# Performance work log

Hardware: AMD Instinct MI355X
Metric: run time of the kernel (lower is better)

The kernel has to match this reference:

```python
import jax, jax.numpy as jnp
import numpy as np

D_MODEL = 1024
N_HEAD = 16
ATT_DIM = D_MODEL // N_HEAD


def setup_inputs() -> dict:
    key = jax.random.key(0)
    ks = jax.random.split(key, 7)
    B, S = 2, 2048
    q = jax.random.normal(ks[0], (B, S, D_MODEL), dtype=jnp.float32)
    k = jax.random.normal(ks[1], (B, S, D_MODEL), dtype=jnp.float32)
    v = jax.random.normal(ks[2], (B, S, D_MODEL), dtype=jnp.float32)
    # per-head projection weights, stored as [H, d_model, att_dim] (x @ W form)
    scale_qkv = float(np.sqrt(6.0 / (D_MODEL + ATT_DIM)))  # xavier_uniform
    Wq = jax.random.uniform(ks[3], (N_HEAD, D_MODEL, ATT_DIM), jnp.float32, -scale_qkv, scale_qkv)
    Wk = jax.random.uniform(ks[4], (N_HEAD, D_MODEL, ATT_DIM), jnp.float32, -scale_qkv, scale_qkv)
    Wv = jax.random.uniform(ks[5], (N_HEAD, D_MODEL, ATT_DIM), jnp.float32, -scale_qkv, scale_qkv)
    scale_o = float(np.sqrt(6.0 / (D_MODEL + D_MODEL)))
    Wo = jax.random.uniform(ks[6], (D_MODEL, D_MODEL), jnp.float32, -scale_o, scale_o)
    return {"q": q, "k": k, "v": v, "Wq": Wq, "Wk": Wk, "Wv": Wv, "Wo": Wo}


def reference(q, k, v, Wq, Wk, Wv, Wo):
    # per-head projections, batched over heads: [H,B,S,E]
    qh = jnp.einsum('bsd,hde->hbse', q, Wq)
    kh = jnp.einsum('bsd,hde->hbse', k, Wk)
    vh = jnp.einsum('bsd,hde->hbse', v, Wv)
    # NOTE: original divides by att_dim (not sqrt(att_dim))
    scores = jnp.einsum('hbqe,hbke->hbqk', qh, kh) / ATT_DIM
    attn = jax.nn.softmax(scores, axis=-1)  # [H,B,Sq,Sk]
    att = jnp.einsum('hbqk,hbke->hbqe', attn, vh)  # [H,B,S,E]
    # concat heads along last dim in head order, then output projection
    H, B, S, E = att.shape
    cat = jnp.transpose(att, (1, 2, 0, 3)).reshape(B, S, H * E)
    out = cat @ Wo  # dropout is identity in eval
    return (out, attn)
```

## Files before the change

### kernel.cpp

```cpp
#include <hip/hip_runtime.h>
#include <hip/hip_bf16.h>

#define DM 1024
#define NH 16
#define AD 64
#define BB 2
#define SS 2048
#define LOG2E 1.44269504f

typedef float f32x4 __attribute__((ext_vector_type(4)));
typedef short bf16x8 __attribute__((ext_vector_type(8)));
typedef unsigned short u16;
typedef unsigned int u32;
typedef u16 u16x4 __attribute__((ext_vector_type(4)));
typedef u16 u16x8 __attribute__((ext_vector_type(8)));
typedef u32 u32x4 __attribute__((ext_vector_type(4)));

static __device__ __forceinline__ u16 f2bf(float f) {
  unsigned u = __builtin_bit_cast(unsigned, f);
  u += 0x7fffu + ((u >> 16) & 1u);
  return (u16)(u >> 16);
}

#define MFMA16(a, b, c) __builtin_amdgcn_mfma_f32_16x16x32_bf16((a), (b), (c), 0, 0, 0)

static __device__ __forceinline__ void ld_lds16(const void* g, void* l) {
  __builtin_amdgcn_global_load_lds((const __attribute__((address_space(1))) u32*)g,
                                   (__attribute__((address_space(3))) u32*)l, 16, 0, 0);
}

#define WAITV(N)                                             \
  do {                                                       \
    asm volatile("s_waitcnt vmcnt(" #N ")" ::: "memory");    \
    __builtin_amdgcn_sched_barrier(0);                       \
  } while (0)
#define WAITL0()                                             \
  do {                                                       \
    asm volatile("s_waitcnt lgkmcnt(0)" ::: "memory");       \
    __builtin_amdgcn_sched_barrier(0);                       \
  } while (0)
#define BAR() __builtin_amdgcn_s_barrier()

#define KFRAG(buf, row, P) (*(const bf16x8*)(&(buf)[(row) * 64 + ((((P) ^ ((row) & 7))) << 3)]))
#define V64(buf, row, P, hh) \
  (*(const u16x4*)(&(buf)[(row) * 64 + ((((P) ^ ((row) & 7))) << 3) + (hh) * 4]))

static __device__ __forceinline__ u32 cvt_pk_bf16(float lo, float hi) {
  u32 r;
  asm("v_cvt_pk_bf16_f32 %0, %1, %2" : "=v"(r) : "v"(lo), "v"(hi));
  return r;
}

__global__ __launch_bounds__(256, 4) void cast3_kernel(const float* __restrict__ s0,
                                                       const float* __restrict__ s1,
                                                       const float* __restrict__ s2,
                                                       u16* __restrict__ d0, u16* __restrict__ d1,
                                                       u16* __restrict__ d2, int n8) {
  const float* src = blockIdx.y == 0 ? s0 : blockIdx.y == 1 ? s1 : s2;
  u16* dst = blockIdx.y == 0 ? d0 : blockIdx.y == 1 ? d1 : d2;
  int i = blockIdx.x * blockDim.x + threadIdx.x;
  int stride = gridDim.x * blockDim.x;
  for (; i < n8; i += stride) {
    const f32x4* p = (const f32x4*)src + 2 * (size_t)i;
    f32x4 a = p[0], b = p[1];
    u16x8 o;
    o[0] = f2bf(a[0]); o[1] = f2bf(a[1]); o[2] = f2bf(a[2]); o[3] = f2bf(a[3]);
    o[4] = f2bf(b[0]); o[5] = f2bf(b[1]); o[6] = f2bf(b[2]); o[7] = f2bf(b[3]);
    *((u16x8*)dst + i) = o;
  }
}

template <int MODE>
__global__ __launch_bounds__(256, 4) void tcast_kernel(const float* __restrict__ s0,
                                                       const float* __restrict__ s1,
                                                       const float* __restrict__ s2,
                                                       u16* __restrict__ dst, int R, int C,
                                                       float scale0) {
  __shared__ float T[64][65];
  const float* src;
  u16* dstp;
  float scale;
  long bo;
  if (MODE == 0) {
    src = s0; bo = (long)blockIdx.z * R * C; dstp = dst; scale = scale0;
  } else {
    int which = blockIdx.z >> 4, zz = blockIdx.z & 15;
    src = which == 0 ? s0 : which == 1 ? s1 : s2;
    bo = (long)zz * R * C;
    dstp = dst + (long)which * NH * R * C;
    scale = which == 0 ? scale0 : 1.0f;
  }
  int r0 = blockIdx.x * 64, c0 = blockIdx.y * 64;
  int cl = threadIdx.x & 63, rl = threadIdx.x >> 6;
#pragma unroll
  for (int i = 0; i < 16; i++) {
    int rr = rl + 4 * i;
    T[cl][rr] = src[bo + (long)(r0 + rr) * C + c0 + cl];
  }
  __syncthreads();
#pragma unroll
  for (int i = 0; i < 16; i++) {
    int cc = rl + 4 * i;
    dstp[bo + (long)(c0 + cc) * R + r0 + cl] = f2bf(T[cc][cl] * scale);
  }
}

__global__ __launch_bounds__(256, 3) void qkvproj_kernel(const u16* __restrict__ X0,
                                                         const u16* __restrict__ WT0,
                                                         u16* __restrict__ out0) {
  __shared__ u16 Ab[2][128 * 64];
  __shared__ u16 Bb[2][64 * 64];
  const long NX = (long)BB * SS * DM;
  const long NW = (long)NH * DM * AD;
  int which = blockIdx.z;
  int sg0 = blockIdx.x * 128;
  int b = sg0 >> 11, s0 = sg0 & (SS - 1);
  int h = blockIdx.y;
  int tid = threadIdx.x, w = tid >> 6, lane = tid & 63, g = lane >> 4, li = lane & 15;
  const u16* xb = X0 + (long)which * NX + ((long)b * SS + s0) * DM;
  const u16* wb = WT0 + (long)which * NW + (long)h * 64 * DM;
  u16* outp = out0 + (long)which * NX;

  const u16* asrc[4];
  u16* adst[2][4];
#pragma unroll
  for (int i = 0; i < 4; i++) {
    int cc = i * 256 + tid;
    int row = cc >> 3, sp = (cc ^ (row & 7)) & 7;
    asrc[i] = xb + (long)row * DM + sp * 8;
    adst[0][i] = &Ab[0][cc * 8];
    adst[1][i] = &Ab[1][cc * 8];
  }
  const u16* bsrc[2];
  u16* bdst[2][2];
#pragma unroll
  for (int i = 0; i < 2; i++) {
    int cc = i * 256 + tid;
    int row = cc >> 3, sp = (cc ^ (row & 7)) & 7;
    bsrc[i] = wb + (long)row * DM + sp * 8;
    bdst[0][i] = &Bb[0][cc * 8];
    bdst[1][i] = &Bb[1][cc * 8];
  }

#pragma unroll
  for (int i = 0; i < 4; i++) ld_lds16(asrc[i], adst[0][i]);
#pragma unroll
  for (int i = 0; i < 2; i++) ld_lds16(bsrc[i], bdst[0][i]);

  f32x4 acc[2][4] = {};
  for (int kc = 0; kc < DM / 64; kc++) {
    int cur = kc & 1;
    if (kc + 1 < DM / 64) {
      int ko = (kc + 1) * 64;
#pragma unroll
      for (int i = 0; i < 4; i++) ld_lds16(asrc[i] + ko, adst[cur ^ 1][i]);
#pragma unroll
      for (int i = 0; i < 2; i++) ld_lds16(bsrc[i] + ko, bdst[cur ^ 1][i]);
      WAITV(6);
    } else {
      WAITV(0);
    }
    BAR();
    const u16* ab = Ab[cur];
    const u16* bb = Bb[cur];
    __builtin_amdgcn_s_setprio(1);
#pragma unroll
    for (int kk = 0; kk < 2; kk++) {
      bf16x8 bf[4];
#pragma unroll
      for (int j = 0; j < 4; j++) bf[j] = KFRAG(bb, j * 16 + li, kk * 4 + g);
#pragma unroll
      for (int mi = 0; mi < 2; mi++) {
        bf16x8 af = KFRAG(ab, w * 32 + mi * 16 + li, kk * 4 + g);
#pragma unroll
        for (int j = 0; j < 4; j++) acc[mi][j] = MFMA16(af, bf[j], acc[mi][j]);
      }
    }
    __builtin_amdgcn_s_setprio(0);
    WAITL0();
    BAR();
  }

  long obase = (long)h * (BB * SS * AD) + (long)b * (SS * AD);
#pragma unroll
  for (int mi = 0; mi < 2; mi++) {
    int sb = s0 + w * 32 + mi * 16 + 4 * g;
#pragma unroll
    for (int j = 0; j < 4; j++) {
      int e = j * 16 + li;
      if (which < 2) {
#pragma unroll
        for (int r = 0; r < 4; r++)
          outp[obase + (long)(sb + r) * AD + e] = f2bf(acc[mi][j][r]);
      } else {
        u16x4 vv;
#pragma unroll
        for (int r = 0; r < 4; r++) vv[r] = f2bf(acc[mi][j][r]);
        *(u16x4*)(outp + obase + (long)e * SS + sb) = vv;
      }
    }
  }
}

__global__ __launch_bounds__(256, 3) void outproj_kernel(const u16* __restrict__ X,
                                                         const u16* __restrict__ WT,
                                                         float* __restrict__ out) {
  __shared__ u16 Ab[2][128 * 64];
  __shared__ u16 Bb[2][64 * 64];
  int sg0 = blockIdx.x * 128;
  int n0 = blockIdx.y * 64;
  int tid = threadIdx.x, w = tid >> 6, lane = tid & 63, g = lane >> 4, li = lane & 15;
  const u16* xb = X + (long)sg0 * DM;
  const u16* wb = WT + (long)n0 * DM;

  const u16* asrc[4];
  u16* adst[2][4];
#pragma unroll
  for (int i = 0; i < 4; i++) {
    int cc = i * 256 + tid;
    int row = cc >> 3, sp = (cc ^ (row & 7)) & 7;
    asrc[i] = xb + (long)row * DM + sp * 8;
    adst[0][i] = &Ab[0][cc * 8];
    adst[1][i] = &Ab[1][cc * 8];
  }
  const u16* bsrc[2];
  u16* bdst[2][2];
#pragma unroll
  for (int i = 0; i < 2; i++) {
    int cc = i * 256 + tid;
    int row = cc >> 3, sp = (cc ^ (row & 7)) & 7;
    bsrc[i] = wb + (long)row * DM + sp * 8;
    bdst[0][i] = &Bb[0][cc * 8];
    bdst[1][i] = &Bb[1][cc * 8];
  }

#pragma unroll
  for (int i = 0; i < 4; i++) ld_lds16(asrc[i], adst[0][i]);
#pragma unroll
  for (int i = 0; i < 2; i++) ld_lds16(bsrc[i], bdst[0][i]);

  f32x4 acc[2][4] = {};
  for (int kc = 0; kc < DM / 64; kc++) {
    int cur = kc & 1;
    if (kc + 1 < DM / 64) {
      int ko = (kc + 1) * 64;
#pragma unroll
      for (int i = 0; i < 4; i++) ld_lds16(asrc[i] + ko, adst[cur ^ 1][i]);
#pragma unroll
      for (int i = 0; i < 2; i++) ld_lds16(bsrc[i] + ko, bdst[cur ^ 1][i]);
      WAITV(6);
    } else {
      WAITV(0);
    }
    BAR();
    const u16* ab = Ab[cur];
    const u16* bb = Bb[cur];
    __builtin_amdgcn_s_setprio(1);
#pragma unroll
    for (int kk = 0; kk < 2; kk++) {
      bf16x8 bf[4];
#pragma unroll
      for (int j = 0; j < 4; j++) bf[j] = KFRAG(bb, j * 16 + li, kk * 4 + g);
#pragma unroll
      for (int mi = 0; mi < 2; mi++) {
        bf16x8 af = KFRAG(ab, w * 32 + mi * 16 + li, kk * 4 + g);
#pragma unroll
        for (int j = 0; j < 4; j++) acc[mi][j] = MFMA16(af, bf[j], acc[mi][j]);
      }
    }
    __builtin_amdgcn_s_setprio(0);
    WAITL0();
    BAR();
  }

#pragma unroll
  for (int mi = 0; mi < 2; mi++) {
    int sb = sg0 + w * 32 + mi * 16 + 4 * g;
#pragma unroll
    for (int j = 0; j < 4; j++) {
      int col = n0 + j * 16 + li;
#pragma unroll
      for (int r = 0; r < 4; r++) out[(long)(sb + r) * DM + col] = acc[mi][j][r];
    }
  }
}

__global__ __launch_bounds__(256, 4) void attn_kernel(const u16* __restrict__ qh,
                                                      const u16* __restrict__ kh,
                                                      const u16* __restrict__ vhT,
                                                      float* __restrict__ attn_out,
                                                      u16* __restrict__ cat) {
  __shared__ u16 Kb[2][64 * 64];
  __shared__ u16 Vb[2][64 * 64];
  int h = blockIdx.y, b = blockIdx.z;
  int hb = h * BB + b;
  int tid = threadIdx.x;
  int w = tid >> 6, lane = tid & 63;
  int g = lane >> 4, li = lane & 15;
  long base = (long)hb * SS * AD;
  const u16* qhb = qh + base;
  const u16* khb = kh + base;
  const u16* vhb = vhT + base;
  int q0 = blockIdx.x * 64 + w * 16;

  bf16x8 bq0 = *(const bf16x8*)(qhb + (q0 + li) * AD + 8 * g);
  bf16x8 bq1 = *(const bf16x8*)(qhb + (q0 + li) * AD + 32 + 8 * g);

  int r1 = tid >> 3, p1 = (tid ^ (r1 & 7)) & 7;
  int r2 = (tid + 256) >> 3, p2 = ((tid + 256) ^ (r2 & 7)) & 7;
  const u16* ks1 = khb + (long)r1 * AD + p1 * 8;
  const u16* ks2 = khb + (long)r2 * AD + p2 * 8;
  const u16* vs1 = vhb + (long)r1 * SS + p1 * 8;
  const u16* vs2 = vhb + (long)r2 * SS + p2 * 8;
  u16* kd0a = &Kb[0][tid * 8]; u16* kd0b = &Kb[0][(tid + 256) * 8];
  u16* kd1a = &Kb[1][tid * 8]; u16* kd1b = &Kb[1][(tid + 256) * 8];
  u16* vd0a = &Vb[0][tid * 8]; u16* vd0b = &Vb[0][(tid + 256) * 8];
  u16* vd1a = &Vb[1][tid * 8]; u16* vd1b = &Vb[1][(tid + 256) * 8];

  float l_run = 0.f;
  ld_lds16(ks1, kd0a); ld_lds16(ks2, kd0b);
  ld_lds16(ks1 + 64 * AD, kd1a); ld_lds16(ks2 + 64 * AD, kd1b);
  ld_lds16(ks1 + 2 * 64 * AD, vd0a); ld_lds16(ks2 + 2 * 64 * AD, vd0b);
  for (int ch4 = 0; ch4 < SS / 64; ch4 += 4) {
#pragma unroll
    for (int u = 0; u < 4; u++) {
      int ch = ch4 + u;
      int slot = (u + 3) & 3;
      u16* pa = slot == 0 ? kd0a : slot == 1 ? kd1a : slot == 2 ? vd0a : vd1a;
      u16* pb = slot == 0 ? kd0b : slot == 1 ? kd1b : slot == 2 ? vd0b : vd1b;
      if (ch + 3 < SS / 64) {
        ld_lds16(ks1 + (ch + 3) * 64 * AD, pa);
        ld_lds16(ks2 + (ch + 3) * 64 * AD, pb);
        WAITV(6);
      } else if (ch == SS / 64 - 3) {
        WAITV(4);
      } else if (ch == SS / 64 - 2) {
        WAITV(2);
      } else {
        WAITV(0);
      }
      BAR();
      const u16* kb = u == 0 ? Kb[0] : u == 1 ? Kb[1] : u == 2 ? Vb[0] : Vb[1];
      f32x4 sacc[4] = {};
      __builtin_amdgcn_s_setprio(1);
#pragma unroll
      for (int mi = 0; mi < 4; mi++) {
        bf16x8 a0 = KFRAG(kb, mi * 16 + li, g);
        bf16x8 a1 = KFRAG(kb, mi * 16 + li, 4 + g);
        sacc[mi] = MFMA16(a0, bq0, sacc[mi]);
        sacc[mi] = MFMA16(a1, bq1, sacc[mi]);
      }
      __builtin_amdgcn_s_setprio(0);
#pragma unroll
      for (int c = 0; c < 4; c++)
#pragma unroll
        for (int r = 0; r < 4; r++) l_run += exp2f(sacc[c][r]);
      WAITL0();
      BAR();
    }
  }
  l_run += __shfl_xor(l_run, 16);
  l_run += __shfl_xor(l_run, 32);
  float moff = log2f(l_run);
  f32x4 minit = {-moff, -moff, -moff, -moff};

  ld_lds16(ks1, kd0a); ld_lds16(ks2, kd0b);
  ld_lds16(vs1, vd0a); ld_lds16(vs2, vd0b);
  f32x4 accv[4] = {};
  float* arow = attn_out + ((long)hb * SS + q0 + li) * SS;
  for (int ch2 = 0; ch2 < SS / 64; ch2 += 2) {
#pragma unroll
    for (int u = 0; u < 2; u++) {
      int ch = ch2 + u;
      u16* kpa = u ? kd0a : kd1a; u16* kpb = u ? kd0b : kd1b;
      u16* vpa = u ? vd0a : vd1a; u16* vpb = u ? vd0b : vd1b;
      if (ch + 1 < SS / 64) {
        ld_lds16(ks1 + (ch + 1) * 64 * AD, kpa);
        ld_lds16(ks2 + (ch + 1) * 64 * AD, kpb);
        ld_lds16(vs1 + (ch + 1) * 64, vpa);
        ld_lds16(vs2 + (ch + 1) * 64, vpb);
        if (ch == 0) {
          WAITV(4);
        } else {
          WAITV(8);
        }
      } else {
        WAITV(4);
      }
      BAR();
      const u16* kb = Kb[u];
      const u16* vb = Vb[u];
      f32x4 sacc[4] = {minit, minit, minit, minit};
      __builtin_amdgcn_s_setprio(1);
#pragma unroll
      for (int mi = 0; mi < 4; mi++) {
        bf16x8 a0 = KFRAG(kb, mi * 16 + li, g);
        bf16x8 a1 = KFRAG(kb, mi * 16 + li, 4 + g);
        sacc[mi] = MFMA16(a0, bq0, sacc[mi]);
        sacc[mi] = MFMA16(a1, bq1, sacc[mi]);
      }
      __builtin_amdgcn_s_setprio(0);
      u32 pw[8];
#pragma unroll
      for (int c = 0; c < 4; c++) {
        f32x4 pv;
#pragma unroll
        for (int r = 0; r < 4; r++) pv[r] = exp2f(sacc[c][r]);
        __builtin_nontemporal_store(pv, (f32x4*)(arow + ch * 64 + c * 16 + 4 * g));
        pw[2 * c] = cvt_pk_bf16(pv[0], pv[1]);
        pw[2 * c + 1] = cvt_pk_bf16(pv[2], pv[3]);
      }
#pragma unroll
      for (int kk = 0; kk < 2; kk++) {
        u32x4 aw = {pw[4 * kk], pw[4 * kk + 1], pw[4 * kk + 2], pw[4 * kk + 3]};
        bf16x8 ap = __builtin_bit_cast(bf16x8, aw);
#pragma unroll
        for (int et = 0; et < 4; et++) {
          int row = et * 16 + li;
          u16x4 b0 = V64(vb, row, 4 * kk + (g >> 1), g & 1);
          u16x4 b1 = V64(vb, row, 4 * kk + 2 + (g >> 1), g & 1);
          u16x8 ub = {b0[0], b0[1], b0[2], b0[3], b1[0], b1[1], b1[2], b1[3]};
          bf16x8 bv = __builtin_bit_cast(bf16x8, ub);
          accv[et] = MFMA16(ap, bv, accv[et]);
        }
      }
      WAITL0();
      BAR();
    }
  }

#pragma unroll
  for (int et = 0; et < 4; et++)
#pragma unroll
    for (int r = 0; r < 4; r++)
      cat[((long)b * SS + q0 + 4 * g + r) * DM + h * AD + et * 16 + li] = f2bf(accv[et][r]);
}

extern "C" void kernel_launch(void* const* d_in, const int* in_sizes, int n_in, void* d_out,
                              int out_size, void* d_ws, size_t ws_size, hipStream_t stream) {
  const float* q = (const float*)d_in[0];
  const float* k = (const float*)d_in[1];
  const float* v = (const float*)d_in[2];
  const float* Wq = (const float*)d_in[3];
  const float* Wk = (const float*)d_in[4];
  const float* Wv = (const float*)d_in[5];
  const float* Wo = (const float*)d_in[6];
  float* out = (float*)d_out;
  float* attn_out = out + (long)BB * SS * DM;

  const long NX = (long)BB * SS * DM;
  const long NW = (long)NH * DM * AD;
  u16* ws = (u16*)d_ws;
  u16* xq = ws;
  u16* xk = xq + NX;
  u16* xv = xk + NX;
  u16* WqT = xv + NX;
  u16* WkT = WqT + NW;
  u16* WvT = WkT + NW;
  u16* WoT = WvT + NW;
  u16* qhw = WoT + (long)DM * DM;
  u16* khw = qhw + NX;
  u16* vhw = khw + NX;
  u16* catw = vhw + NX;

  (void)xk; (void)xv; (void)WkT; (void)WvT;

  cast3_kernel<<<dim3(700, 3), 256, 0, stream>>>(q, k, v, xq, xk, xv, (int)(NX / 8));
  tcast_kernel<1><<<dim3(16, 1, 48), 256, 0, stream>>>(Wq, Wk, Wv, WqT, DM, AD, LOG2E / AD);
  tcast_kernel<0><<<dim3(16, 16, 1), 256, 0, stream>>>(Wo, nullptr, nullptr, WoT, DM, DM, 1.0f);

  qkvproj_kernel<<<dim3(BB * SS / 128, NH, 3), 256, 0, stream>>>(xq, WqT, qhw);

  attn_kernel<<<dim3(SS / 64, NH, BB), 256, 0, stream>>>(qhw, khw, vhw, attn_out, catw);

  outproj_kernel<<<dim3(BB * SS / 128, DM / 64), 256, 0, stream>>>(catw, WoT, out);
}
```

Baseline: 260.5 us.

## Fuse prep kernels, reorder attention grid, split sum accumulators, drop nontemporal stores

Merges the three input-cast and weight-transpose launches into one prep kernel that picks its work from the flat block index, removing two launches. The attention grid now puts head*batch in x and query tile in y, so blocks that run at the same time share K/V for the same head. The softmax-denominator sum uses four independent accumulators to shorten the dependency chain. The attention-probability stores become ordinary stores instead of nontemporal ones, which changes cache behaviour for the large output write.

```diff
diff --git a/kernel.cpp b/kernel.cpp
--- a/kernel.cpp
+++ b/kernel.cpp
@@ -51,47 +51,59 @@
   return r;
 }
 
-__global__ __launch_bounds__(256, 4) void cast3_kernel(const float* __restrict__ s0,
-                                                       const float* __restrict__ s1,
-                                                       const float* __restrict__ s2,
-                                                       u16* __restrict__ d0, u16* __restrict__ d1,
-                                                       u16* __restrict__ d2, int n8) {
-  const float* src = blockIdx.y == 0 ? s0 : blockIdx.y == 1 ? s1 : s2;
-  u16* dst = blockIdx.y == 0 ? d0 : blockIdx.y == 1 ? d1 : d2;
-  int i = blockIdx.x * blockDim.x + threadIdx.x;
-  int stride = gridDim.x * blockDim.x;
-  for (; i < n8; i += stride) {
-    const f32x4* p = (const f32x4*)src + 2 * (size_t)i;
-    f32x4 a = p[0], b = p[1];
-    u16x8 o;
-    o[0] = f2bf(a[0]); o[1] = f2bf(a[1]); o[2] = f2bf(a[2]); o[3] = f2bf(a[3]);
-    o[4] = f2bf(b[0]); o[5] = f2bf(b[1]); o[6] = f2bf(b[2]); o[7] = f2bf(b[3]);
-    *((u16x8*)dst + i) = o;
-  }
-}
-
-template <int MODE>
-__global__ __launch_bounds__(256, 4) void tcast_kernel(const float* __restrict__ s0,
-                                                       const float* __restrict__ s1,
-                                                       const float* __restrict__ s2,
-                                                       u16* __restrict__ dst, int R, int C,
-                                                       float scale0) {
+__global__ __launch_bounds__(256, 4) void prep_kernel(const float* __restrict__ q,
+                                                      const float* __restrict__ k,
+                                                      const float* __restrict__ v,
+                                                      const float* __restrict__ Wq,
+                                                      const float* __restrict__ Wk,
+                                                      const float* __restrict__ Wv,
+                                                      const float* __restrict__ Wo,
+                                                      u16* __restrict__ xq,
+                                                      u16* __restrict__ WqT,
+                                                      u16* __restrict__ WoT) {
   __shared__ float T[64][65];
+  const long NX = (long)BB * SS * DM;
+  int id = blockIdx.x;
+  int tid = threadIdx.x;
+  if (id < 2100) {
+    int tensor = id / 700, xi = id - tensor * 700;
+    const float* src = tensor == 0 ? q : tensor == 1 ? k : v;
+    u16* dst = xq + (long)tensor * NX;
+    int n8 = (int)(NX / 8);
+    int stride = 700 * 256;
+    for (int i = xi * 256 + tid; i < n8; i += stride) {
+      const f32x4* p = (const f32x4*)src + 2 * (size_t)i;
+      f32x4 a = p[0], b = p[1];
+      u16x8 o;
+      o[0] = f2bf(a[0]); o[1] = f2bf(a[1]); o[2] = f2bf(a[2]); o[3] = f2bf(a[3]);
+      o[4] = f2bf(b[0]); o[5] = f2bf(b[1]); o[6] = f2bf(b[2]); o[7] = f2bf(b[3]);
+      *((u16x8*)dst + i) = o;
+    }
+    return;
+  }
   const float* src;
   u16* dstp;
   float scale;
   long bo;
-  if (MODE == 0) {
-    src = s0; bo = (long)blockIdx.z * R * C; dstp = dst; scale = scale0;
+  int R, C, r0, c0;
+  if (id < 2868) {
+    int flat = id - 2100;
+    int x = flat & 15, z = flat >> 4;
+    int which = z >> 4, zz = z & 15;
+    src = which == 0 ? Wq : which == 1 ? Wk : Wv;
+    R = DM; C = AD;
+    bo = (long)zz * R * C;
+    dstp = WqT + (long)which * NH * R * C;
+    scale = which == 0 ? (LOG2E / AD) : 1.0f;
+    r0 = x * 64; c0 = 0;
   } else {
-    int which = blockIdx.z >> 4, zz = blockIdx.z & 15;
-    src = which == 0 ? s0 : which == 1 ? s1 : s2;
-    bo = (long)zz * R * C;
-    dstp = dst + (long)which * NH * R * C;
-    scale = which == 0 ? scale0 : 1.0f;
-  }
-  int r0 = blockIdx.x * 64, c0 = blockIdx.y * 64;
-  int cl = threadIdx.x & 63, rl = threadIdx.x >> 6;
+    int flat = id - 2868;
+    int x = flat & 15, yb = flat >> 4;
+    src = Wo; dstp = WoT; scale = 1.0f;
+    R = DM; C = DM; bo = 0;
+    r0 = x * 64; c0 = yb * 64;
+  }
+  int cl = tid & 63, rl = tid >> 6;
 #pragma unroll
   for (int i = 0; i < 16; i++) {
     int rr = rl + 4 * i;
@@ -292,8 +304,8 @@
                                                       u16* __restrict__ cat) {
   __shared__ u16 Kb[2][64 * 64];
   __shared__ u16 Vb[2][64 * 64];
-  int h = blockIdx.y, b = blockIdx.z;
-  int hb = h * BB + b;
+  int hb = blockIdx.x;
+  int h = hb >> 1, b = hb & 1;
   int tid = threadIdx.x;
   int w = tid >> 6, lane = tid & 63;
   int g = lane >> 4, li = lane & 15;
@@ -301,7 +313,7 @@
   const u16* qhb = qh + base;
   const u16* khb = kh + base;
   const u16* vhb = vhT + base;
-  int q0 = blockIdx.x * 64 + w * 16;
+  int q0 = blockIdx.y * 64 + w * 16;
 
   bf16x8 bq0 = *(const bf16x8*)(qhb + (q0 + li) * AD + 8 * g);
   bf16x8 bq1 = *(const bf16x8*)(qhb + (q0 + li) * AD + 32 + 8 * g);
@@ -317,7 +329,7 @@
   u16* vd0a = &Vb[0][tid * 8]; u16* vd0b = &Vb[0][(tid + 256) * 8];
   u16* vd1a = &Vb[1][tid * 8]; u16* vd1b = &Vb[1][(tid + 256) * 8];
 
-  float l_run = 0.f;
+  f32x4 l4 = {0.f, 0.f, 0.f, 0.f};
   ld_lds16(ks1, kd0a); ld_lds16(ks2, kd0b);
   ld_lds16(ks1 + 64 * AD, kd1a); ld_lds16(ks2 + 64 * AD, kd1b);
   ld_lds16(ks1 + 2 * 64 * AD, vd0a); ld_lds16(ks2 + 2 * 64 * AD, vd0b);
@@ -354,11 +366,12 @@
 #pragma unroll
       for (int c = 0; c < 4; c++)
 #pragma unroll
-        for (int r = 0; r < 4; r++) l_run += exp2f(sacc[c][r]);
+        for (int r = 0; r < 4; r++) l4[r] += exp2f(sacc[c][r]);
       WAITL0();
       BAR();
     }
   }
+  float l_run = (l4[0] + l4[1]) + (l4[2] + l4[3]);
   l_run += __shfl_xor(l_run, 16);
   l_run += __shfl_xor(l_run, 32);
   float moff = log2f(l_run);
@@ -406,7 +419,7 @@
         f32x4 pv;
 #pragma unroll
         for (int r = 0; r < 4; r++) pv[r] = exp2f(sacc[c][r]);
-        __builtin_nontemporal_store(pv, (f32x4*)(arow + ch * 64 + c * 16 + 4 * g));
+        *(f32x4*)(arow + ch * 64 + c * 16 + 4 * g) = pv;
         pw[2 * c] = cvt_pk_bf16(pv[0], pv[1]);
         pw[2 * c + 1] = cvt_pk_bf16(pv[2], pv[3]);
       }
@@ -465,13 +478,11 @@
 
   (void)xk; (void)xv; (void)WkT; (void)WvT;
 
-  cast3_kernel<<<dim3(700, 3), 256, 0, stream>>>(q, k, v, xq, xk, xv, (int)(NX / 8));
-  tcast_kernel<1><<<dim3(16, 1, 48), 256, 0, stream>>>(Wq, Wk, Wv, WqT, DM, AD, LOG2E / AD);
-  tcast_kernel<0><<<dim3(16, 16, 1), 256, 0, stream>>>(Wo, nullptr, nullptr, WoT, DM, DM, 1.0f);
+  prep_kernel<<<3124, 256, 0, stream>>>(q, k, v, Wq, Wk, Wv, Wo, xq, WqT, WoT);
 
   qkvproj_kernel<<<dim3(BB * SS / 128, NH, 3), 256, 0, stream>>>(xq, WqT, qhw);
 
-  attn_kernel<<<dim3(SS / 64, NH, BB), 256, 0, stream>>>(qhw, khw, vhw, attn_out, catw);
+  attn_kernel<<<dim3(NH * BB, SS / 64), 256, 0, stream>>>(qhw, khw, vhw, attn_out, catw);
 
   outproj_kernel<<<dim3(BB * SS / 128, DM / 64), 256, 0, stream>>>(catw, WoT, out);
 }
```

Result: no change. 260.7 us (+0.1%).
